# Kernel tuning notes

Hardware: AMD Instinct MI355X
Metric: run time of the kernel (lower is better)

The kernel has to match this reference:

```python
import jax, jax.numpy as jnp
import numpy as np

B, S, H = 2, 1024, 1024          # batch, seq, hidden_size
KD, NH, K = 128, 8, 8            # key_dims, num_heads, top-k
NE = 65536                       # num_experts (perfect square)
NK = 256                         # num_keys = sqrt(num_experts)
EPS = 1e-5                       # BatchNorm eps


def setup_inputs() -> dict:
    key = jax.random.key(0)
    ks = jax.random.split(key, 5)
    inputs = jax.random.normal(ks[0], (B, S, H), jnp.float32)
    bn_gamma = jnp.ones((H,), jnp.float32)
    bn_beta = jnp.zeros((H,), jnp.float32)
    # nn.Linear default init scale ~ 1/sqrt(fan_in)
    w_q = jax.random.normal(ks[1], (2 * NH * KD, H), jnp.float32) * (1.0 / np.sqrt(H))
    keys_p = jax.random.normal(ks[2], (NH, NK, 2, KD), jnp.float32) * 0.02
    lim = float(np.sqrt(6.0 / (NE + H)))  # xavier_uniform
    down = jax.random.uniform(ks[3], (NE, H), jnp.float32, -lim, lim)
    up = jax.random.uniform(ks[4], (NE, H), jnp.float32, -lim, lim)
    return {"inputs": inputs, "bn_gamma": bn_gamma, "bn_beta": bn_beta,
            "w_q": w_q, "keys_p": keys_p, "down": down, "up": up}


def reference(inputs, bn_gamma, bn_beta, w_q, keys_p, down, up):
    b, s, d = inputs.shape
    # BatchNorm1d over flattened (b*s, d), training-mode batch stats (biased var)
    x = inputs.reshape(b * s, d)
    mean = x.mean(axis=0)
    var = x.var(axis=0)
    xn = (x - mean) * jax.lax.rsqrt(var + EPS) * bn_gamma + bn_beta
    xn = xn.reshape(b, s, d)
    # queries: Linear -> unflatten to (b,s,2,h,kd) -> permute to (2,b,s,h,kd)
    q = (xn @ w_q.T).reshape(b, s, 2, NH, KD).transpose(2, 0, 1, 3, 4)
    # similarity against product keys: (2,b,s,h,NK)
    sim = jnp.einsum('pbnhd,hkpd->pbnhk', q, keys_p)
    scores, idx = jax.lax.top_k(sim, K)               # (2,b,s,h,K)
    # cartesian combine of the two sub-key top-k lists -> (b,s,h,K*K)
    all_scores = (scores[0][..., :, None] + scores[1][..., None, :]).reshape(b, s, NH, K * K)
    all_idx = (idx[0][..., :, None] * NK + idx[1][..., None, :]).reshape(b, s, NH, K * K)
    sc, pk = jax.lax.top_k(all_scores, K)             # (b,s,h,K)
    indices = jnp.take_along_axis(all_idx, pk, axis=-1)
    # expert retrieval: gather per-token expert weight vectors
    wd = down[indices]                                # (b,s,h,K,d)
    hmid = jnp.einsum('bnd,bnhkd->bnhk', inputs, wd)
    hmid = jax.nn.sigmoid(sc) * jax.nn.gelu(hmid, approximate=False)
    wu = up[indices]                                  # (b,s,h,K,d)
    return jnp.einsum('bnhk,bnhkd->bnd', hmid, wu)
```

## Files before the change

### kernel.cpp

```cpp
#include <hip/hip_runtime.h>
#include <hip/hip_bf16.h>
#include <math.h>

#define HDIM 1024
#define TOK 2048
#define NHEAD 8
#define KD 128
#define NKEY 256
#define KSEL 8
#define BN_EPS 1e-5f

typedef _Float16 half8 __attribute__((ext_vector_type(8)));
typedef float floatx4 __attribute__((ext_vector_type(4)));

__device__ __forceinline__ uint32_t pack_f16pair(float v) {
    _Float16 h = (_Float16)v;
    float hf = (float)h;
    _Float16 l = (_Float16)((v - hf) * 2048.0f);
    return (uint32_t)__builtin_bit_cast(unsigned short, h) |
           ((uint32_t)__builtin_bit_cast(unsigned short, l) << 16);
}

__global__ __launch_bounds__(256) void bn_partial_k(const float* __restrict__ x,
                                                    float* __restrict__ psum,
                                                    float* __restrict__ psq) {
    int b = blockIdx.x;
    int t = threadIdx.x;
    float s[4] = {0.f, 0.f, 0.f, 0.f};
    float s2[4] = {0.f, 0.f, 0.f, 0.f};
    int r0 = b * 32;
    for (int r = 0; r < 32; ++r) {
        const float* row = x + (size_t)(r0 + r) * HDIM;
#pragma unroll
        for (int j = 0; j < 4; ++j) {
            float v = row[t + j * 256];
            s[j] += v;
            s2[j] += v * v;
        }
    }
#pragma unroll
    for (int j = 0; j < 4; ++j) {
        psum[b * HDIM + t + j * 256] = s[j];
        psq[b * HDIM + t + j * 256] = s2[j];
    }
}

__global__ __launch_bounds__(256) void bn_final_k(const float* __restrict__ psum,
                                                  const float* __restrict__ psq,
                                                  const float* __restrict__ gamma,
                                                  const float* __restrict__ beta,
                                                  float* __restrict__ scale,
                                                  float* __restrict__ shift) {
    int c = blockIdx.x * 256 + threadIdx.x;
    float s = 0.f, s2 = 0.f;
    for (int b = 0; b < 64; ++b) {
        s += psum[b * HDIM + c];
        s2 += psq[b * HDIM + c];
    }
    float mean = s * (1.0f / TOK);
    float var = s2 * (1.0f / TOK) - mean * mean;
    float sc = gamma[c] * rsqrtf(var + BN_EPS);
    scale[c] = sc;
    shift[c] = beta[c] - mean * sc;
}

template <int NORM>
__global__ __launch_bounds__(256) void cvt_pack_k(const float* __restrict__ in,
                                                  uint32_t* __restrict__ out,
                                                  const float* __restrict__ sc,
                                                  const float* __restrict__ sh) {
    int i = (blockIdx.x * 256 + threadIdx.x) * 4;
    float4 v = *(const float4*)(in + i);
    if (NORM) {
        int c = i & 1023;
        float4 s4 = *(const float4*)(sc + c);
        float4 h4 = *(const float4*)(sh + c);
        v.x = fmaf(v.x, s4.x, h4.x);
        v.y = fmaf(v.y, s4.y, h4.y);
        v.z = fmaf(v.z, s4.z, h4.z);
        v.w = fmaf(v.w, s4.w, h4.w);
    }
    uint4 o;
    o.x = pack_f16pair(v.x);
    o.y = pack_f16pair(v.y);
    o.z = pack_f16pair(v.z);
    o.w = pack_f16pair(v.w);
    *(uint4*)(out + i) = o;
}

__global__ __launch_bounds__(256) void cvt_keys_k(const float* __restrict__ in,
                                                  uint32_t* __restrict__ out) {
    int i = blockIdx.x * 256 + threadIdx.x;
    int d = i & 127;
    int nk = (i >> 7) & 255;
    int hp = i >> 15;
    int h = hp >> 1, p = hp & 1;
    out[i] = pack_f16pair(in[h * 65536 + nk * 256 + p * 128 + d]);
}

template <int MODE>
__global__ __launch_bounds__(512) void mgemm_k(const uint32_t* __restrict__ A,
                                               const uint32_t* __restrict__ B,
                                               float* __restrict__ Cf,
                                               uint32_t* __restrict__ Cp) {
    __shared__ _Float16 Ah[128][40];
    __shared__ _Float16 Al[128][40];
    __shared__ _Float16 Bh[128][40];
    __shared__ _Float16 Bl[128][40];

    const int tid = threadIdx.x;
    const int m0 = blockIdx.x * 128;
    const int n0 = blockIdx.y * 128;

    const uint32_t* Ab;
    const uint32_t* Bb;
    int lda, ldb, NS, ldc;
    size_t cbase;
    if (MODE == 0) {
        lda = 1024; ldb = 1024; NS = 32; ldc = 2048; cbase = 0;
        Ab = A; Bb = B;
    } else {
        lda = 2048; ldb = 128; NS = 4; ldc = 4096;
        int z = blockIdx.z, p = z >> 3, h = z & 7;
        Ab = A + p * 1024 + h * 128;
        Bb = B + (size_t)(h * 2 + p) * 32768;
        cbase = p * 2048 + h * 256;
    }

    const int st = tid & 255;
    const int srow = st >> 1;
    const int skh = (st & 1) * 16;
    const bool isB = (tid >= 256);
    const uint32_t* sp = (isB ? (Bb + (size_t)(n0 + srow) * ldb)
                              : (Ab + (size_t)(m0 + srow) * lda)) + skh;
    _Float16* Hp = isB ? &Bh[srow][skh] : &Ah[srow][skh];
    _Float16* Lp = isB ? &Bl[srow][skh] : &Al[srow][skh];

    const int w = tid >> 6, lane = tid & 63;
    const int wm = w >> 2, wn = w & 3;
    const int fr = lane & 15, kg = lane >> 4;

    floatx4 acc1[4][2];
    floatx4 acc2[4][2];
#pragma unroll
    for (int i = 0; i < 4; ++i)
#pragma unroll
        for (int j = 0; j < 2; ++j) {
            acc1[i][j] = (floatx4)0.0f;
            acc2[i][j] = (floatx4)0.0f;
        }

    uint32_t rg[16];
    auto gload = [&](int s) {
        const uint32_t* p = sp + s * 32;
#pragma unroll
        for (int j = 0; j < 4; ++j) *(uint4*)&rg[j * 4] = *(const uint4*)(p + j * 4);
    };
    auto lwrite = [&]() {
        uint32_t hh[8], ll[8];
#pragma unroll
        for (int j = 0; j < 8; ++j) {
            hh[j] = __builtin_amdgcn_perm(rg[2 * j + 1], rg[2 * j], 0x05040100u);
            ll[j] = __builtin_amdgcn_perm(rg[2 * j + 1], rg[2 * j], 0x07060302u);
        }
        *(uint4*)(Hp) = *(uint4*)&hh[0];
        *(uint4*)(Hp + 8) = *(uint4*)&hh[4];
        *(uint4*)(Lp) = *(uint4*)&ll[0];
        *(uint4*)(Lp + 8) = *(uint4*)&ll[4];
    };

    gload(0);
    lwrite();
    for (int s = 0; s < NS; ++s) {
        if (s + 1 < NS) gload(s + 1);
        __syncthreads();
        half8 ah[4], al[4], bh2[2], bl2[2];
#pragma unroll
        for (int mf = 0; mf < 4; ++mf) {
            int r = wm * 64 + mf * 16 + fr;
            ah[mf] = *(const half8*)&Ah[r][kg * 8];
            al[mf] = *(const half8*)&Al[r][kg * 8];
        }
#pragma unroll
        for (int nf = 0; nf < 2; ++nf) {
            int r = wn * 32 + nf * 16 + fr;
            bh2[nf] = *(const half8*)&Bh[r][kg * 8];
            bl2[nf] = *(const half8*)&Bl[r][kg * 8];
        }
#pragma unroll
        for (int mf = 0; mf < 4; ++mf)
#pragma unroll
            for (int nf = 0; nf < 2; ++nf) {
                acc1[mf][nf] = __builtin_amdgcn_mfma_f32_16x16x32_f16(ah[mf], bh2[nf], acc1[mf][nf], 0, 0, 0);
                acc2[mf][nf] = __builtin_amdgcn_mfma_f32_16x16x32_f16(ah[mf], bl2[nf], acc2[mf][nf], 0, 0, 0);
                acc2[mf][nf] = __builtin_amdgcn_mfma_f32_16x16x32_f16(al[mf], bh2[nf], acc2[mf][nf], 0, 0, 0);
            }
        __syncthreads();
        if (s + 1 < NS) lwrite();
    }

#pragma unroll
    for (int mf = 0; mf < 4; ++mf)
#pragma unroll
        for (int nf = 0; nf < 2; ++nf)
#pragma unroll
            for (int r = 0; r < 4; ++r) {
                float q = acc1[mf][nf][r] + acc2[mf][nf][r] * (1.0f / 2048.0f);
                int row = m0 + wm * 64 + mf * 16 + kg * 4 + r;
                int col = n0 + wn * 32 + nf * 16 + fr;
                if (MODE == 0)
                    Cp[(size_t)row * 2048 + col] = pack_f16pair(q);
                else
                    Cf[cbase + (size_t)row * (size_t)ldc + col] = q;
            }
}

__global__ __launch_bounds__(512) void topk_k(const float* __restrict__ sim,
                                              int* __restrict__ eidx,
                                              float* __restrict__ gates) {
    int t = blockIdx.x;
    int h = threadIdx.x >> 6;
    int lane = threadIdx.x & 63;
    const float* s0p = sim + (size_t)t * 4096 + h * 256;
    const float* s1p = s0p + 2048;
    float4 v0 = *(const float4*)(s0p + lane * 4);
    float4 v1 = *(const float4*)(s1p + lane * 4);
    float c0[4] = {v0.x, v0.y, v0.z, v0.w};
    float c1[4] = {v1.x, v1.y, v1.z, v1.w};

    float tv0[8], tv1[8];
    int ti0[8], ti1[8];

#pragma unroll
    for (int r = 0; r < 8; ++r) {
        float bv = c0[0];
        int bi = lane * 4;
#pragma unroll
        for (int j = 1; j < 4; ++j)
            if (c0[j] > bv) { bv = c0[j]; bi = lane * 4 + j; }
#pragma unroll
        for (int off = 1; off < 64; off <<= 1) {
            float ov = __shfl_xor(bv, off);
            int oi = __shfl_xor(bi, off);
            if (ov > bv || (ov == bv && oi < bi)) { bv = ov; bi = oi; }
        }
        tv0[r] = bv;
        ti0[r] = bi;
        if ((bi >> 2) == lane) {
            int jj = bi & 3;
#pragma unroll
            for (int q = 0; q < 4; ++q)
                if (q == jj) c0[q] = -INFINITY;
        }
    }
#pragma unroll
    for (int r = 0; r < 8; ++r) {
        float bv = c1[0];
        int bi = lane * 4;
#pragma unroll
        for (int j = 1; j < 4; ++j)
            if (c1[j] > bv) { bv = c1[j]; bi = lane * 4 + j; }
#pragma unroll
        for (int off = 1; off < 64; off <<= 1) {
            float ov = __shfl_xor(bv, off);
            int oi = __shfl_xor(bi, off);
            if (ov > bv || (ov == bv && oi < bi)) { bv = ov; bi = oi; }
        }
        tv1[r] = bv;
        ti1[r] = bi;
        if ((bi >> 2) == lane) {
            int jj = bi & 3;
#pragma unroll
            for (int q = 0; q < 4; ++q)
                if (q == jj) c1[q] = -INFINITY;
        }
    }

    int ii = lane >> 3, jj = lane & 7;
    float a = -INFINITY, b = -INFINITY;
#pragma unroll
    for (int r = 0; r < 8; ++r) {
        if (ii == r) a = tv0[r];
        if (jj == r) b = tv1[r];
    }
    float cv = a + b;
    int cpos = lane;

    int outbase = (t * NHEAD + h) * KSEL;
#pragma unroll
    for (int r = 0; r < 8; ++r) {
        float bv = cv;
        int bp = cpos;
#pragma unroll
        for (int off = 1; off < 64; off <<= 1) {
            float ov = __shfl_xor(bv, off);
            int op = __shfl_xor(bp, off);
            if (ov > bv || (ov == bv && op < bp)) { bv = ov; bp = op; }
        }
        if (lane == 0) {
            int pi = bp >> 3, pj = bp & 7;
            int e0 = 0, e1 = 0;
#pragma unroll
            for (int q = 0; q < 8; ++q) {
                if (pi == q) e0 = ti0[q];
                if (pj == q) e1 = ti1[q];
            }
            eidx[outbase + r] = e0 * NKEY + e1;
            gates[outbase + r] = 1.0f / (1.0f + expf(-bv));
        }
        if (lane == bp) cv = -INFINITY;
    }
}

__global__ __launch_bounds__(512, 2) void expert_k(const float* __restrict__ x,
                                                   const float* __restrict__ down,
                                                   const float* __restrict__ up,
                                                   const int* __restrict__ eidx,
                                                   const float* __restrict__ gates,
                                                   float* __restrict__ out) {
    int t = blockIdx.x;
    int w = threadIdx.x >> 6;
    int lane = threadIdx.x & 63;
    __shared__ __align__(16) float4 accs[8][256];

    const float4* x4 = (const float4*)(x + (size_t)t * HDIM);
    float4 xv[4];
#pragma unroll
    for (int j = 0; j < 4; ++j) xv[j] = x4[lane + 64 * j];

    int base = t * 64 + w * 8;
    int e[8];
    float g[8];
#pragma unroll
    for (int i = 0; i < 8; ++i) {
        e[i] = eidx[base + i];
        g[i] = gates[base + i];
    }

    float dot[8];
#pragma unroll
    for (int i = 0; i < 8; ++i) dot[i] = 0.f;
#pragma unroll
    for (int i = 0; i < 8; ++i) {
        const float4* d = (const float4*)(down + (size_t)e[i] * HDIM);
#pragma unroll
        for (int j = 0; j < 4; ++j) {
            float4 dv = d[lane + 64 * j];
            dot[i] += xv[j].x * dv.x + xv[j].y * dv.y + xv[j].z * dv.z + xv[j].w * dv.w;
        }
    }

#pragma unroll
    for (int off = 32; off >= 1; off >>= 1) {
#pragma unroll
        for (int i = 0; i < 8; ++i) dot[i] += __shfl_xor(dot[i], off);
    }
    float hm[8];
#pragma unroll
    for (int i = 0; i < 8; ++i) {
        float d = dot[i];
        hm[i] = g[i] * 0.5f * d * (1.0f + erff(d * 0.70710678118654752f));
    }

    float4 acc[4];
#pragma unroll
    for (int j = 0; j < 4; ++j) acc[j] = make_float4(0.f, 0.f, 0.f, 0.f);
#pragma unroll
    for (int i = 0; i < 8; ++i) {
        const float4* u = (const float4*)(up + (size_t)e[i] * HDIM);
        float h = hm[i];
#pragma unroll
        for (int j = 0; j < 4; ++j) {
            float4 uv = u[lane + 64 * j];
            acc[j].x = fmaf(h, uv.x, acc[j].x);
            acc[j].y = fmaf(h, uv.y, acc[j].y);
            acc[j].z = fmaf(h, uv.z, acc[j].z);
            acc[j].w = fmaf(h, uv.w, acc[j].w);
        }
    }

#pragma unroll
    for (int j = 0; j < 4; ++j) accs[w][lane + 64 * j] = acc[j];
    __syncthreads();
    if (threadIdx.x < 256) {
        int s = threadIdx.x;
        float4 o = accs[0][s];
#pragma unroll
        for (int ww = 1; ww < 8; ++ww) {
            float4 r = accs[ww][s];
            o.x += r.x; o.y += r.y; o.z += r.z; o.w += r.w;
        }
        ((float4*)(out + (size_t)t * HDIM))[s] = o;
    }
}

extern "C" void kernel_launch(void* const* d_in, const int* in_sizes, int n_in,
                              void* d_out, int out_size, void* d_ws, size_t ws_size,
                              hipStream_t stream) {
    const float* x = (const float*)d_in[0];
    const float* gamma = (const float*)d_in[1];
    const float* beta = (const float*)d_in[2];
    const float* w_q = (const float*)d_in[3];
    const float* keys = (const float*)d_in[4];
    const float* down = (const float*)d_in[5];
    const float* up = (const float*)d_in[6];
    float* out = (float*)d_out;
    float* ws = (float*)d_ws;

    float* psum = ws;
    float* psq = ws + 65536;
    float* scale = ws + 131072;
    float* shift = ws + 132096;
    int* eidx = (int*)(ws + 133120);
    float* gates = ws + 264192;
    uint32_t* xpk = (uint32_t*)(ws + 524288);
    uint32_t* wpk = (uint32_t*)(ws + 2621440);
    float* sim = ws + 524288;
    uint32_t* kpk = (uint32_t*)(ws + 8912896);
    uint32_t* qpk = (uint32_t*)(ws + 9437184);

    bn_partial_k<<<64, 256, 0, stream>>>(x, psum, psq);
    bn_final_k<<<4, 256, 0, stream>>>(psum, psq, gamma, beta, scale, shift);

    cvt_pack_k<1><<<2048, 256, 0, stream>>>(x, xpk, scale, shift);
    cvt_pack_k<0><<<2048, 256, 0, stream>>>(w_q, wpk, nullptr, nullptr);
    cvt_keys_k<<<2048, 256, 0, stream>>>(keys, kpk);

    mgemm_k<0><<<dim3(16, 16, 1), 512, 0, stream>>>(xpk, wpk, nullptr, qpk);
    mgemm_k<1><<<dim3(16, 2, 16), 512, 0, stream>>>(qpk, kpk, sim, nullptr);

    topk_k<<<2048, 512, 0, stream>>>(sim, eidx, gates);
    expert_k<<<2048, 512, 0, stream>>>(x, down, up, eidx, gates, out);
}
```

Baseline: 285.7 us.

## Fuse BN normalization and fp16 split conversion into GEMM tile loads

Removes the three standalone conversion kernels (normalized x pack, w_q pack, keys pack). The GEMM kernels now load fp32 directly, apply the BatchNorm scale/shift for the activation operand, and split into high/low fp16 halves while writing shared memory. This drops three launches and the round trip of packed intermediates through global memory. In exchange the conversion is repeated for every tile that reuses an operand, and the extra scale/shift loads and arithmetic add register pressure inside the GEMM loop.

```diff
diff --git a/kernel.cpp b/kernel.cpp
--- a/kernel.cpp
+++ b/kernel.cpp
@@ -64,45 +64,14 @@
     shift[c] = beta[c] - mean * sc;
 }
 
-template <int NORM>
-__global__ __launch_bounds__(256) void cvt_pack_k(const float* __restrict__ in,
-                                                  uint32_t* __restrict__ out,
-                                                  const float* __restrict__ sc,
-                                                  const float* __restrict__ sh) {
-    int i = (blockIdx.x * 256 + threadIdx.x) * 4;
-    float4 v = *(const float4*)(in + i);
-    if (NORM) {
-        int c = i & 1023;
-        float4 s4 = *(const float4*)(sc + c);
-        float4 h4 = *(const float4*)(sh + c);
-        v.x = fmaf(v.x, s4.x, h4.x);
-        v.y = fmaf(v.y, s4.y, h4.y);
-        v.z = fmaf(v.z, s4.z, h4.z);
-        v.w = fmaf(v.w, s4.w, h4.w);
-    }
-    uint4 o;
-    o.x = pack_f16pair(v.x);
-    o.y = pack_f16pair(v.y);
-    o.z = pack_f16pair(v.z);
-    o.w = pack_f16pair(v.w);
-    *(uint4*)(out + i) = o;
-}
-
-__global__ __launch_bounds__(256) void cvt_keys_k(const float* __restrict__ in,
-                                                  uint32_t* __restrict__ out) {
-    int i = blockIdx.x * 256 + threadIdx.x;
-    int d = i & 127;
-    int nk = (i >> 7) & 255;
-    int hp = i >> 15;
-    int h = hp >> 1, p = hp & 1;
-    out[i] = pack_f16pair(in[h * 65536 + nk * 256 + p * 128 + d]);
-}
-
 template <int MODE>
-__global__ __launch_bounds__(512) void mgemm_k(const uint32_t* __restrict__ A,
-                                               const uint32_t* __restrict__ B,
+__global__ __launch_bounds__(512) void mgemm_k(const float* __restrict__ Af,
+                                               const uint32_t* __restrict__ Apk,
+                                               const float* __restrict__ Bf,
                                                float* __restrict__ Cf,
-                                               uint32_t* __restrict__ Cp) {
+                                               uint32_t* __restrict__ Cp,
+                                               const float* __restrict__ scale,
+                                               const float* __restrict__ shift) {
     __shared__ _Float16 Ah[128][40];
     __shared__ _Float16 Al[128][40];
     __shared__ _Float16 Bh[128][40];
@@ -112,27 +81,27 @@
     const int m0 = blockIdx.x * 128;
     const int n0 = blockIdx.y * 128;
 
-    const uint32_t* Ab;
-    const uint32_t* Bb;
-    int lda, ldb, NS, ldc;
-    size_t cbase;
-    if (MODE == 0) {
-        lda = 1024; ldb = 1024; NS = 32; ldc = 2048; cbase = 0;
-        Ab = A; Bb = B;
-    } else {
-        lda = 2048; ldb = 128; NS = 4; ldc = 4096;
-        int z = blockIdx.z, p = z >> 3, h = z & 7;
-        Ab = A + p * 1024 + h * 128;
-        Bb = B + (size_t)(h * 2 + p) * 32768;
-        cbase = p * 2048 + h * 256;
-    }
-
     const int st = tid & 255;
     const int srow = st >> 1;
     const int skh = (st & 1) * 16;
     const bool isB = (tid >= 256);
-    const uint32_t* sp = (isB ? (Bb + (size_t)(n0 + srow) * ldb)
-                              : (Ab + (size_t)(m0 + srow) * lda)) + skh;
+
+    int NS;
+    const float* spf = nullptr;
+    const uint32_t* spp = nullptr;
+    size_t cbase = 0;
+    if (MODE == 0) {
+        NS = 32;
+        spf = (isB ? (Bf + (size_t)(n0 + srow) * 1024)
+                   : (Af + (size_t)(m0 + srow) * 1024)) + skh;
+    } else {
+        NS = 4;
+        int z = blockIdx.z, p = z >> 3, h = z & 7;
+        if (isB) spf = Bf + (size_t)h * 65536 + (size_t)(n0 + srow) * 256 + p * 128 + skh;
+        else     spp = Apk + (size_t)(m0 + srow) * 2048 + p * 1024 + h * 128 + skh;
+        cbase = (size_t)(p * 2048 + h * 256);
+    }
+
     _Float16* Hp = isB ? &Bh[srow][skh] : &Ah[srow][skh];
     _Float16* Lp = isB ? &Bl[srow][skh] : &Al[srow][skh];
 
@@ -150,27 +119,57 @@
             acc2[i][j] = (floatx4)0.0f;
         }
 
-    uint32_t rg[16];
+    float rf[16];
+    uint32_t rp[16];
+
     auto gload = [&](int s) {
-        const uint32_t* p = sp + s * 32;
-#pragma unroll
-        for (int j = 0; j < 4; ++j) *(uint4*)&rg[j * 4] = *(const uint4*)(p + j * 4);
+        if (MODE == 1 && !isB) {
+            const uint32_t* p = spp + s * 32;
+#pragma unroll
+            for (int j = 0; j < 4; ++j) *(uint4*)&rp[j * 4] = *(const uint4*)(p + j * 4);
+        } else {
+            const float* p = spf + s * 32;
+#pragma unroll
+            for (int j = 0; j < 4; ++j) *(float4*)&rf[j * 4] = *(const float4*)(p + j * 4);
+        }
     };
-    auto lwrite = [&]() {
-        uint32_t hh[8], ll[8];
-#pragma unroll
-        for (int j = 0; j < 8; ++j) {
-            hh[j] = __builtin_amdgcn_perm(rg[2 * j + 1], rg[2 * j], 0x05040100u);
-            ll[j] = __builtin_amdgcn_perm(rg[2 * j + 1], rg[2 * j], 0x07060302u);
+    auto lwrite = [&](int s) {
+        __align__(16) _Float16 hh[16], ll[16];
+        if (MODE == 1 && !isB) {
+#pragma unroll
+            for (int j = 0; j < 8; ++j) {
+                uint32_t hw = __builtin_amdgcn_perm(rp[2 * j + 1], rp[2 * j], 0x05040100u);
+                uint32_t lw = __builtin_amdgcn_perm(rp[2 * j + 1], rp[2 * j], 0x07060302u);
+                *(uint32_t*)&hh[2 * j] = hw;
+                *(uint32_t*)&ll[2 * j] = lw;
+            }
+        } else {
+            float sv[16], hv[16];
+            if (MODE == 0 && !isB) {
+                const int c0 = s * 32 + skh;
+#pragma unroll
+                for (int jj = 0; jj < 4; ++jj) {
+                    *(float4*)&sv[jj * 4] = *(const float4*)(scale + c0 + jj * 4);
+                    *(float4*)&hv[jj * 4] = *(const float4*)(shift + c0 + jj * 4);
+                }
+            }
+#pragma unroll
+            for (int j = 0; j < 16; ++j) {
+                float v = rf[j];
+                if (MODE == 0 && !isB) v = fmaf(v, sv[j], hv[j]);
+                _Float16 h = (_Float16)v;
+                hh[j] = h;
+                ll[j] = (_Float16)((v - (float)h) * 2048.0f);
+            }
         }
         *(uint4*)(Hp) = *(uint4*)&hh[0];
-        *(uint4*)(Hp + 8) = *(uint4*)&hh[4];
+        *(uint4*)(Hp + 8) = *(uint4*)&hh[8];
         *(uint4*)(Lp) = *(uint4*)&ll[0];
-        *(uint4*)(Lp + 8) = *(uint4*)&ll[4];
+        *(uint4*)(Lp + 8) = *(uint4*)&ll[8];
     };
 
     gload(0);
-    lwrite();
+    lwrite(0);
     for (int s = 0; s < NS; ++s) {
         if (s + 1 < NS) gload(s + 1);
         __syncthreads();
@@ -196,7 +195,7 @@
                 acc2[mf][nf] = __builtin_amdgcn_mfma_f32_16x16x32_f16(al[mf], bh2[nf], acc2[mf][nf], 0, 0, 0);
             }
         __syncthreads();
-        if (s + 1 < NS) lwrite();
+        if (s + 1 < NS) lwrite(s + 1);
     }
 
 #pragma unroll
@@ -211,7 +210,7 @@
                 if (MODE == 0)
                     Cp[(size_t)row * 2048 + col] = pack_f16pair(q);
                 else
-                    Cf[cbase + (size_t)row * (size_t)ldc + col] = q;
+                    Cf[cbase + (size_t)row * 4096 + col] = q;
             }
 }
 
@@ -413,21 +412,16 @@
     float* shift = ws + 132096;
     int* eidx = (int*)(ws + 133120);
     float* gates = ws + 264192;
-    uint32_t* xpk = (uint32_t*)(ws + 524288);
-    uint32_t* wpk = (uint32_t*)(ws + 2621440);
-    float* sim = ws + 524288;
-    uint32_t* kpk = (uint32_t*)(ws + 8912896);
-    uint32_t* qpk = (uint32_t*)(ws + 9437184);
+    uint32_t* qpk = (uint32_t*)(ws + 524288);
+    float* sim = ws + 4718592;
 
     bn_partial_k<<<64, 256, 0, stream>>>(x, psum, psq);
     bn_final_k<<<4, 256, 0, stream>>>(psum, psq, gamma, beta, scale, shift);
 
-    cvt_pack_k<1><<<2048, 256, 0, stream>>>(x, xpk, scale, shift);
-    cvt_pack_k<0><<<2048, 256, 0, stream>>>(w_q, wpk, nullptr, nullptr);
-    cvt_keys_k<<<2048, 256, 0, stream>>>(keys, kpk);
-
-    mgemm_k<0><<<dim3(16, 16, 1), 512, 0, stream>>>(xpk, wpk, nullptr, qpk);
-    mgemm_k<1><<<dim3(16, 2, 16), 512, 0, stream>>>(qpk, kpk, sim, nullptr);
+    mgemm_k<0><<<dim3(16, 16, 1), 512, 0, stream>>>(x, nullptr, w_q, nullptr, qpk,
+                                                    scale, shift);
+    mgemm_k<1><<<dim3(16, 2, 16), 512, 0, stream>>>(nullptr, qpk, keys, sim, nullptr,
+                                                    nullptr, nullptr);
 
     topk_k<<<2048, 512, 0, stream>>>(sim, eidx, gates);
     expert_k<<<2048, 512, 0, stream>>>(x, down, up, eidx, gates, out);
```

Result: slower. 302.9 us (+6.0%).
